# Kernel optimization log

Hardware: AMD Instinct MI355X
Metric: run time of the kernel (lower is better)

The kernel has to match this reference:

```python
import jax, jax.numpy as jnp
import numpy as np

B, N, H, NH, HD, DE = 4, 512, 512, 8, 64, 64
DFF = 4 * H
EPS = 1e-5


def setup_inputs() -> dict:
    key = jax.random.key(0)
    ks = jax.random.split(key, 32)
    w = lambda k, *s: jax.random.normal(k, s, jnp.float32) * 0.02
    inp = {}
    inp['messages'] = jax.random.normal(ks[0], (B, N, H), jnp.float32)
    inp['distance_matrix'] = jax.random.randint(ks[1], (B, N, N), 0, 201).astype(jnp.float32)
    mask = jax.random.randint(ks[2], (B, N, N), 0, 2).astype(jnp.float32)
    inp['mask'] = jnp.maximum(mask, jnp.eye(N, dtype=jnp.float32)[None])  # ensure diag visible
    inp['emb_table'] = w(ks[3], 201, DE)
    inp['Wdq'] = w(ks[4], H, DE); inp['bdq'] = jnp.zeros((H,), jnp.float32)
    inp['Wdk'] = w(ks[5], H, DE); inp['bdk'] = jnp.zeros((H,), jnp.float32)
    inp['Wq'] = w(ks[6], H, H);   inp['bq'] = jnp.zeros((H,), jnp.float32)
    inp['Wk'] = w(ks[7], H, H);   inp['bk'] = jnp.zeros((H,), jnp.float32)
    inp['Wv'] = w(ks[8], H, H);   inp['bv'] = jnp.zeros((H,), jnp.float32)
    inp['Wo'] = w(ks[9], H, H);   inp['bo'] = jnp.zeros((H,), jnp.float32)
    inp['W_ih'] = w(ks[10], 3 * H, H); inp['b_ih'] = jnp.zeros((3 * H,), jnp.float32)
    inp['W_hh'] = w(ks[11], 3 * H, H); inp['b_hh'] = jnp.zeros((3 * H,), jnp.float32)
    inp['W1'] = w(ks[12], DFF, H); inp['b1'] = jnp.zeros((DFF,), jnp.float32)
    inp['W2'] = w(ks[13], H, DFF); inp['b2'] = jnp.zeros((H,), jnp.float32)
    inp['g2'] = jnp.ones((H,), jnp.float32); inp['beta2'] = jnp.zeros((H,), jnp.float32)
    return inp


def reference(messages, distance_matrix, mask, emb_table, Wdq, bdq, Wdk, bdk,
              Wq, bq, Wk, bk, Wv, bv, Wo, bo, W_ih, b_ih, W_hh, b_hh,
              W1, b1, W2, b2, g2, beta2):
    # distance embedding lookup (B,N,N,DE)
    idx = jnp.clip(distance_matrix.astype(jnp.int32), 0, 200)
    emb = emb_table[idx]
    # mean over dim then linear == linear then mean (linear maps commute with mean)
    dq = jnp.mean(emb, axis=2) @ Wdq.T + bdq  # (B,N,H)
    dk = jnp.mean(emb, axis=1) @ Wdk.T + bdk  # (B,N,H)
    Q = ((messages + dq) @ Wq.T + bq).reshape(B, N, NH, HD).transpose(0, 2, 1, 3)
    K = ((messages + dk) @ Wk.T + bk).reshape(B, N, NH, HD).transpose(0, 2, 1, 3)
    V = (messages @ Wv.T + bv).reshape(B, N, NH, HD).transpose(0, 2, 1, 3)
    scale = 1.0 / np.sqrt(HD).astype(np.float32)
    scores = jnp.einsum('bhnd,bhmd->bhnm', Q, K) * scale
    scores = jnp.where(mask[:, None] == 0, -jnp.inf, scores)
    aw = jax.nn.softmax(scores, axis=-1)
    ao = jnp.einsum('bhnm,bhmd->bhnd', aw, V).transpose(0, 2, 1, 3).reshape(B, N, H)
    ao = ao @ Wo.T + bo
    # GRUCell: x = attn output, h = messages
    gx = ao @ W_ih.T + b_ih
    gh = messages @ W_hh.T + b_hh
    xr, xz, xn = jnp.split(gx, 3, axis=-1)
    hr, hz, hn = jnp.split(gh, 3, axis=-1)
    r = jax.nn.sigmoid(xr + hr)
    z = jax.nn.sigmoid(xz + hz)
    n = jnp.tanh(xn + r * hn)
    u = (1.0 - z) * n + z * messages
    # FFN + residual + LayerNorm
    f = jax.nn.relu(u @ W1.T + b1) @ W2.T + b2
    y = u + f
    mu = jnp.mean(y, axis=-1, keepdims=True)
    var = jnp.var(y, axis=-1, keepdims=True)
    return (y - mu) / jnp.sqrt(var + EPS) * g2 + beta2
```

## Files before the change

### kernel.cpp

```cpp
#include <hip/hip_runtime.h>
#include <hip/hip_bf16.h>
#include <math.h>

#define Bz 4
#define Nn 512
#define Hh 512
#define NHh 8
#define HDd 64
#define DEe 64
#define DFFf 2048
#define EPSs 1e-5f
#define QS 1536
#define GS 3072

typedef __attribute__((ext_vector_type(8))) short bf16x8;
typedef __attribute__((ext_vector_type(4))) short bf16x4;
typedef __attribute__((ext_vector_type(4))) float f32x4;

__device__ inline short f2bf(float x) {
    unsigned u = __builtin_bit_cast(unsigned, x);
    unsigned r = (u + 0x7FFFu + ((u >> 16) & 1u)) >> 16;
    return (short)r;
}
__device__ inline float b2f(unsigned short u) {
    unsigned v = ((unsigned)u) << 16;
    return __builtin_bit_cast(float, v);
}
__device__ inline void gld16(const void* g, void* l) {
    __builtin_amdgcn_global_load_lds(
        (const __attribute__((address_space(1))) void*)g,
        (__attribute__((address_space(3))) void*)l, 16, 0, 0);
}

struct CvtArgs {
    const float* src[11];
    unsigned short* dst[11];
    int n[11];
};
__global__ __launch_bounds__(256) void cvttr_kernel(
    CvtArgs a, const float* __restrict__ dist, float* __restrict__ distT)
{
    __shared__ float T[64][68];
    int t = threadIdx.x;
    if (blockIdx.x < 512) {
        for (int sg = 0; sg < 11; ++sg) {
            const float4* s = (const float4*)a.src[sg];
            ushort4* d = (ushort4*)a.dst[sg];
            int n4 = a.n[sg] >> 2;
            for (int i = blockIdx.x * 256 + t; i < n4; i += 512 * 256) {
                float4 v = s[i];
                ushort4 o = {(unsigned short)f2bf(v.x), (unsigned short)f2bf(v.y),
                             (unsigned short)f2bf(v.z), (unsigned short)f2bf(v.w)};
                d[i] = o;
            }
        }
    } else {
        int tid = blockIdx.x - 512;
        int b = tid >> 6;
        int i0 = ((tid >> 3) & 7) * 64, j0 = (tid & 7) * 64;
        int rr = t >> 4, c4 = (t & 15) * 4;
#pragma unroll
        for (int p = 0; p < 4; ++p) {
            int r = rr + p * 16;
            float4 v = *(const float4*)&dist[((size_t)(b * Nn + i0 + r)) * Nn + j0 + c4];
            *(float4*)&T[r][c4] = v;
        }
        __syncthreads();
#pragma unroll
        for (int p = 0; p < 4; ++p) {
            int jr = rr + p * 16;
            float4 v = {T[c4 + 0][jr], T[c4 + 1][jr], T[c4 + 2][jr], T[c4 + 3][jr]};
            *(float4*)&distT[((size_t)(b * Nn + j0 + jr)) * Nn + i0 + c4] = v;
        }
    }
}

__global__ __launch_bounds__(256) void dmean2_kernel(
    const float* __restrict__ dist, const float* __restrict__ distT,
    const float* __restrict__ emb,
    unsigned short* __restrict__ dqe, unsigned short* __restrict__ dke)
{
    int bi = blockIdx.x;
    const float* src = blockIdx.y ? distT : dist;
    unsigned short* out = blockIdx.y ? dke : dqe;
    int t = threadIdx.x;
    int d = t & 63;
    int g = t >> 6;
    const float* drow = src + (size_t)bi * Nn + g * 128;
    float acc = 0.f;
#pragma unroll 4
    for (int it = 0; it < 32; ++it) {
        float4 v = *(const float4*)(drow + it * 4);
        int i0 = min(max((int)v.x, 0), 200);
        int i1 = min(max((int)v.y, 0), 200);
        int i2 = min(max((int)v.z, 0), 200);
        int i3 = min(max((int)v.w, 0), 200);
        acc += emb[i0 * DEe + d];
        acc += emb[i1 * DEe + d];
        acc += emb[i2 * DEe + d];
        acc += emb[i3 * DEe + d];
    }
    __shared__ float red[4][64];
    red[g][d] = acc;
    __syncthreads();
    if (g == 0) {
        float s = red[0][d] + red[1][d] + red[2][d] + red[3][d];
        out[(size_t)bi * DEe + d] = (unsigned short)f2bf(s * (1.0f / Nn));
    }
}

struct SegArgs {
    const unsigned short* A[3];
    int lda[3];
    const float* bias[3];
    const void* res[3];
    int rlda;
};

template<int BM, int BN, int RELU, int RESM, int OUTF>
__global__ __launch_bounds__(256) void mgf_kernel(
    SegArgs sa, const unsigned short* __restrict__ W,
    void* __restrict__ C, int K, int SW, int ldc)
{
    constexpr int WM = BM / 2, WN = BN / 2;
    constexpr int MT = WM / 16, NT = WN / 16;
    constexpr int IPA = BM / 32, IPB = BN / 32;
    __shared__ unsigned short As[2][BM * 64];
    __shared__ unsigned short Bs[2][BN * 64];
    int t = threadIdx.x, lane = t & 63, wid = t >> 6;
    int wm = wid >> 1, wn = wid & 1;
    int m0 = blockIdx.y * BM, n0 = blockIdx.x * BN;
    int seg = n0 / SW;
    int segbase = seg * SW;
    const unsigned short* A = sa.A[seg];
    int lda = sa.lda[seg];
    int lrow8 = lane >> 3;
    int lunit = (lane & 7) ^ lrow8;

    f32x4 acc[MT][NT] = {};

    auto stage = [&](int buf, int kt) {
#pragma unroll
        for (int i = 0; i < IPA; ++i) {
            int c = wid * IPA + i;
            gld16(A + (size_t)(m0 + c * 8 + lrow8) * lda + kt + lunit * 8,
                  &As[buf][c * 512]);
        }
#pragma unroll
        for (int i = 0; i < IPB; ++i) {
            int c = wid * IPB + i;
            gld16(W + (size_t)(n0 + c * 8 + lrow8) * K + kt + lunit * 8,
                  &Bs[buf][c * 512]);
        }
    };

    stage(0, 0);
    __syncthreads();
    int cur = 0;
    for (int kt = 0; kt < K; kt += 64) {
        if (kt + 64 < K) stage(cur ^ 1, kt + 64);
#pragma unroll
        for (int kk = 0; kk < 2; ++kk) {
            bf16x8 fa[MT], fb[NT];
            int ub = kk * 4 + (lane >> 4);
#pragma unroll
            for (int mt = 0; mt < MT; ++mt) {
                int r = wm * WM + mt * 16 + (lane & 15);
                fa[mt] = *(const bf16x8*)&As[cur][r * 64 + ((ub ^ (r & 7)) << 3)];
            }
#pragma unroll
            for (int nt = 0; nt < NT; ++nt) {
                int r = wn * WN + nt * 16 + (lane & 15);
                fb[nt] = *(const bf16x8*)&Bs[cur][r * 64 + ((ub ^ (r & 7)) << 3)];
            }
#pragma unroll
            for (int mt = 0; mt < MT; ++mt)
#pragma unroll
                for (int nt = 0; nt < NT; ++nt)
                    acc[mt][nt] = __builtin_amdgcn_mfma_f32_16x16x32_bf16(
                        fa[mt], fb[nt], acc[mt][nt], 0, 0, 0);
        }
        __syncthreads();
        cur ^= 1;
    }

    int cr = (lane >> 4) * 4, ccl = lane & 15;
#pragma unroll
    for (int mt = 0; mt < MT; ++mt) {
#pragma unroll
        for (int nt = 0; nt < NT; ++nt) {
            int col = n0 + wn * WN + nt * 16 + ccl;
            int lcol = col - segbase;
            float bv = sa.bias[seg][lcol];
#pragma unroll
            for (int r = 0; r < 4; ++r) {
                int row = m0 + wm * WM + mt * 16 + cr + r;
                float o = acc[mt][nt][r] + bv;
                if (RESM == 1)
                    o += ((const float*)sa.res[seg])[(size_t)row * sa.rlda + lcol];
                if (RESM == 2)
                    o += b2f(((const unsigned short*)sa.res[seg])
                                 [(size_t)row * sa.rlda + lcol]);
                if (RELU) o = fmaxf(o, 0.f);
                if (OUTF)
                    ((float*)C)[(size_t)row * ldc + col] = o;
                else
                    ((unsigned short*)C)[(size_t)row * ldc + col] =
                        (unsigned short)f2bf(o);
            }
        }
    }
}

__global__ __launch_bounds__(256) void attn_mfma_kernel(
    const unsigned short* __restrict__ QKV, const float* __restrict__ mask,
    unsigned short* __restrict__ AO)
{
    __shared__ unsigned short Qs[64 * 64];
    __shared__ unsigned short Ks[64 * 64];
    __shared__ unsigned short Vt[64 * 64];
    __shared__ float Ms[64 * 65];
    __shared__ unsigned short Pl[4][16 * 72];

    int t = threadIdx.x;
    int lane = t & 63;
    int wq = t >> 6;
    int g = lane >> 4, cc = lane & 15;
    int q0 = blockIdx.x * 64;
    int h = blockIdx.y, b = blockIdx.z;

    int lr = t >> 2;
    int u0 = (t & 3) * 2;
    int c0f = (t & 3) * 16;

    {
        const unsigned short* src =
            QKV + ((size_t)(b * Nn + q0 + lr)) * QS + h * HDd + u0 * 8;
        bf16x8 p0 = *(const bf16x8*)(src);
        bf16x8 p1 = *(const bf16x8*)(src + 8);
        *(bf16x8*)&Qs[lr * 64 + ((u0 ^ (lr & 7)) << 3)] = p0;
        *(bf16x8*)&Qs[lr * 64 + (((u0 + 1) ^ (lr & 7)) << 3)] = p1;
    }

    const unsigned short* Krow =
        QKV + ((size_t)(b * Nn + lr)) * QS + 512 + h * HDd + u0 * 8;
    int vkey = t >> 4;
    int vd0 = (t & 15) * 4;
    const unsigned short* Vbase =
        QKV + ((size_t)(b * Nn)) * QS + 1024 + h * HDd + vd0;
    const float* Mrow = mask + ((size_t)(b * Nn + q0 + lr)) * Nn + c0f;

    bf16x8 kr0, kr1;
    ushort4 vr[4];
    float4 mreg[4];
    auto issue = [&](int kc) {
        int k0 = kc * 64;
        const unsigned short* kp = Krow + (size_t)k0 * QS;
        kr0 = *(const bf16x8*)(kp);
        kr1 = *(const bf16x8*)(kp + 8);
        const float* mp = Mrow + k0;
        mreg[0] = *(const float4*)(mp);
        mreg[1] = *(const float4*)(mp + 4);
        mreg[2] = *(const float4*)(mp + 8);
        mreg[3] = *(const float4*)(mp + 12);
#pragma unroll
        for (int p = 0; p < 4; ++p)
            vr[p] = *(const ushort4*)(Vbase + (size_t)(k0 + vkey + p * 16) * QS);
    };
    issue(0);
    __syncthreads();

    bf16x8 qf0 = *(bf16x8*)&Qs[(wq * 16 + cc) * 64 + (((0 * 4 + g) ^ (cc & 7)) << 3)];
    bf16x8 qf1 = *(bf16x8*)&Qs[(wq * 16 + cc) * 64 + (((1 * 4 + g) ^ (cc & 7)) << 3)];

    const float scale = 0.125f;
    float m_run = -1e30f, l_run = 0.f;
    f32x4 o[4] = {};

    for (int kc = 0; kc < 8; ++kc) {
        {
            *(bf16x8*)&Ks[lr * 64 + ((u0 ^ (lr & 7)) << 3)] = kr0;
            *(bf16x8*)&Ks[lr * 64 + (((u0 + 1) ^ (lr & 7)) << 3)] = kr1;

            float* msr = &Ms[lr * 65 + c0f];
            msr[0] = mreg[0].x;  msr[1] = mreg[0].y;  msr[2] = mreg[0].z;  msr[3] = mreg[0].w;
            msr[4] = mreg[1].x;  msr[5] = mreg[1].y;  msr[6] = mreg[1].z;  msr[7] = mreg[1].w;
            msr[8] = mreg[2].x;  msr[9] = mreg[2].y;  msr[10] = mreg[2].z; msr[11] = mreg[2].w;
            msr[12] = mreg[3].x; msr[13] = mreg[3].y; msr[14] = mreg[3].z; msr[15] = mreg[3].w;

#pragma unroll
            for (int p = 0; p < 4; ++p) {
                int key = vkey + p * 16;
                unsigned short vals[4] = {vr[p].x, vr[p].y, vr[p].z, vr[p].w};
#pragma unroll
                for (int jj = 0; jj < 4; ++jj) {
                    int j = (jj + (t >> 2)) & 3;
                    int d = vd0 + j;
                    Vt[d * 64 + (key ^ ((d & 7) << 3))] = vals[j];
                }
            }
        }
        __syncthreads();
        if (kc < 7) issue(kc + 1);

        f32x4 s[4] = {};
#pragma unroll
        for (int kt = 0; kt < 4; ++kt) {
            int rA = kt * 16 + cc;
            bf16x8 a0 = *(bf16x8*)&Ks[rA * 64 + (((0 * 4 + g) ^ (rA & 7)) << 3)];
            s[kt] = __builtin_amdgcn_mfma_f32_16x16x32_bf16(a0, qf0, s[kt], 0, 0, 0);
            bf16x8 a1 = *(bf16x8*)&Ks[rA * 64 + (((1 * 4 + g) ^ (rA & 7)) << 3)];
            s[kt] = __builtin_amdgcn_mfma_f32_16x16x32_bf16(a1, qf1, s[kt], 0, 0, 0);
        }

        float pv[4][4];
        float tmax = -1e30f;
#pragma unroll
        for (int kt = 0; kt < 4; ++kt) {
#pragma unroll
            for (int r = 0; r < 4; ++r) {
                float mv = Ms[(wq * 16 + cc) * 65 + kt * 16 + g * 4 + r];
                float svv = (mv == 0.f) ? -1e30f : s[kt][r];
                pv[kt][r] = svv;
                tmax = fmaxf(tmax, svv);
            }
        }
        tmax = fmaxf(tmax, __shfl_xor(tmax, 16));
        tmax = fmaxf(tmax, __shfl_xor(tmax, 32));
        float mnew = fmaxf(m_run, tmax);
        float rescale = __expf((m_run - mnew) * scale);
        float psum = 0.f;
#pragma unroll
        for (int kt = 0; kt < 4; ++kt) {
#pragma unroll
            for (int r = 0; r < 4; ++r) {
                float sv = pv[kt][r];
                float p = (sv == -1e30f) ? 0.f : __expf((sv - mnew) * scale);
                pv[kt][r] = p;
                psum += p;
            }
        }
        psum += __shfl_xor(psum, 16);
        psum += __shfl_xor(psum, 32);
        l_run = l_run * rescale + psum;
        m_run = mnew;
#pragma unroll
        for (int dt = 0; dt < 4; ++dt) {
            o[dt][0] *= rescale; o[dt][1] *= rescale;
            o[dt][2] *= rescale; o[dt][3] *= rescale;
        }

#pragma unroll
        for (int kt = 0; kt < 4; ++kt) {
            bf16x4 pk = {f2bf(pv[kt][0]), f2bf(pv[kt][1]),
                         f2bf(pv[kt][2]), f2bf(pv[kt][3])};
            *(bf16x4*)&Pl[wq][cc * 72 + kt * 16 + g * 4] = pk;
        }
        bf16x8 pf0 = *(bf16x8*)&Pl[wq][cc * 72 + 0 + g * 8];
        bf16x8 pf1 = *(bf16x8*)&Pl[wq][cc * 72 + 32 + g * 8];

#pragma unroll
        for (int dt = 0; dt < 4; ++dt) {
            int rV = dt * 16 + cc;
            bf16x8 vf0 = *(bf16x8*)&Vt[rV * 64 + (((0 * 4 + g) ^ (rV & 7)) << 3)];
            o[dt] = __builtin_amdgcn_mfma_f32_16x16x32_bf16(vf0, pf0, o[dt], 0, 0, 0);
            bf16x8 vf1 = *(bf16x8*)&Vt[rV * 64 + (((1 * 4 + g) ^ (rV & 7)) << 3)];
            o[dt] = __builtin_amdgcn_mfma_f32_16x16x32_bf16(vf1, pf1, o[dt], 0, 0, 0);
        }
        __syncthreads();
    }

    float invl = 1.f / l_run;
#pragma unroll
    for (int dt = 0; dt < 4; ++dt) {
        ushort4 w = {(unsigned short)f2bf(o[dt][0] * invl),
                     (unsigned short)f2bf(o[dt][1] * invl),
                     (unsigned short)f2bf(o[dt][2] * invl),
                     (unsigned short)f2bf(o[dt][3] * invl)};
        *(ushort4*)&AO[((size_t)(b * Nn + q0 + wq * 16 + cc)) * Hh +
                       h * HDd + dt * 16 + g * 4] = w;
    }
}

__global__ __launch_bounds__(256) void gru_kernel(
    const unsigned short* __restrict__ G,
    const float* __restrict__ msg, unsigned short* __restrict__ u)
{
    int i4 = blockIdx.x * 256 + threadIdx.x;
    int e = i4 * 4;
    int row = e >> 9, col = e & 511;
    const unsigned short* gxr = G + (size_t)row * GS;
    const unsigned short* ghr = gxr + 1536;
    ushort4 xr4 = *(const ushort4*)(gxr + col);
    ushort4 xz4 = *(const ushort4*)(gxr + col + 512);
    ushort4 xn4 = *(const ushort4*)(gxr + col + 1024);
    ushort4 hr4 = *(const ushort4*)(ghr + col);
    ushort4 hz4 = *(const ushort4*)(ghr + col + 512);
    ushort4 hn4 = *(const ushort4*)(ghr + col + 1024);
    float4 mg4 = *(const float4*)(msg + e);
    float mv[4] = {mg4.x, mg4.y, mg4.z, mg4.w};
    unsigned short xr[4] = {xr4.x, xr4.y, xr4.z, xr4.w};
    unsigned short xz[4] = {xz4.x, xz4.y, xz4.z, xz4.w};
    unsigned short xn[4] = {xn4.x, xn4.y, xn4.z, xn4.w};
    unsigned short hr[4] = {hr4.x, hr4.y, hr4.z, hr4.w};
    unsigned short hz[4] = {hz4.x, hz4.y, hz4.z, hz4.w};
    unsigned short hn[4] = {hn4.x, hn4.y, hn4.z, hn4.w};
    ushort4 out;
    unsigned short* op = (unsigned short*)&out;
#pragma unroll
    for (int j = 0; j < 4; ++j) {
        float r = 1.f / (1.f + __expf(-(b2f(xr[j]) + b2f(hr[j]))));
        float z = 1.f / (1.f + __expf(-(b2f(xz[j]) + b2f(hz[j]))));
        float n = tanhf(b2f(xn[j]) + r * b2f(hn[j]));
        op[j] = (unsigned short)f2bf((1.f - z) * n + z * mv[j]);
    }
    *(ushort4*)(u + e) = out;
}

__global__ __launch_bounds__(256) void ln_kernel(
    const float* __restrict__ Y, const float* __restrict__ g,
    const float* __restrict__ be, float* __restrict__ out)
{
    int row = blockIdx.x, t = threadIdx.x;
    const float* yr = Y + (size_t)row * Hh;
    float v0 = yr[t], v1 = yr[t + 256];
    float s = v0 + v1, s2 = v0 * v0 + v1 * v1;
#pragma unroll
    for (int o = 1; o < 64; o <<= 1) {
        s += __shfl_xor(s, o);
        s2 += __shfl_xor(s2, o);
    }
    __shared__ float rs[4], rs2[4];
    int w = t >> 6;
    if ((t & 63) == 0) { rs[w] = s; rs2[w] = s2; }
    __syncthreads();
    float ts = rs[0] + rs[1] + rs[2] + rs[3];
    float ts2 = rs2[0] + rs2[1] + rs2[2] + rs2[3];
    float mu = ts * (1.0f / Hh);
    float var = ts2 * (1.0f / Hh) - mu * mu;
    float rstd = rsqrtf(var + EPSs);
    out[(size_t)row * Hh + t] = (v0 - mu) * rstd * g[t] + be[t];
    out[(size_t)row * Hh + t + 256] = (v1 - mu) * rstd * g[t + 256] + be[t + 256];
}

extern "C" void kernel_launch(void* const* d_in, const int* in_sizes, int n_in,
                              void* d_out, int out_size, void* d_ws, size_t ws_size,
                              hipStream_t stream) {
    const float* messages = (const float*)d_in[0];
    const float* dist     = (const float*)d_in[1];
    const float* mask     = (const float*)d_in[2];
    const float* emb      = (const float*)d_in[3];
    const float* Wdq = (const float*)d_in[4];  const float* bdq = (const float*)d_in[5];
    const float* Wdk = (const float*)d_in[6];  const float* bdk = (const float*)d_in[7];
    const float* Wq  = (const float*)d_in[8];  const float* bq  = (const float*)d_in[9];
    const float* Wk  = (const float*)d_in[10]; const float* bk  = (const float*)d_in[11];
    const float* Wv  = (const float*)d_in[12]; const float* bv  = (const float*)d_in[13];
    const float* Wo  = (const float*)d_in[14]; const float* bo  = (const float*)d_in[15];
    const float* W_ih = (const float*)d_in[16]; const float* b_ih = (const float*)d_in[17];
    const float* W_hh = (const float*)d_in[18]; const float* b_hh = (const float*)d_in[19];
    const float* W1  = (const float*)d_in[20]; const float* b1  = (const float*)d_in[21];
    const float* W2  = (const float*)d_in[22]; const float* b2  = (const float*)d_in[23];
    const float* g2  = (const float*)d_in[24]; const float* beta2 = (const float*)d_in[25];

    const int M = Bz * Nn;
    char* ws = (char*)d_ws;

    unsigned short* wdqb = (unsigned short*)(ws + 0);
    unsigned short* wdkb = (unsigned short*)(ws + 65536);
    unsigned short* wqkv = (unsigned short*)(ws + 131072);
    unsigned short* wob  = (unsigned short*)(ws + 1703936);
    unsigned short* wgate= (unsigned short*)(ws + 2228224);
    unsigned short* w1b  = (unsigned short*)(ws + 5373952);
    unsigned short* w2b  = (unsigned short*)(ws + 7471104);
    unsigned short* msgs = (unsigned short*)(ws + 9568256);
    unsigned short* dqe  = (unsigned short*)(ws + 11665408);
    unsigned short* dke  = (unsigned short*)(ws + 11927552);
    unsigned short* XQXK = (unsigned short*)(ws + 12189696);
    unsigned short* QKVb = (unsigned short*)(ws + 16384000);
    unsigned short* AO   = (unsigned short*)(ws + 22675456);
    unsigned short* aob  = (unsigned short*)(ws + 24772608);
    unsigned short* G    = (unsigned short*)(ws + 26869760);
    unsigned short* ub   = (unsigned short*)(ws + 39452672);
    unsigned short* f1   = (unsigned short*)(ws + 41549824);
    float*          yb   = (float*)(ws + 49938432);
    float*          distT= (float*)(ws + 54132736);

    dim3 blk(256);

    CvtArgs ca;
    ca.src[0] = messages; ca.dst[0] = msgs; ca.n[0] = M * Hh;
    ca.src[1] = Wdq;  ca.dst[1] = wdqb;          ca.n[1] = Hh * DEe;
    ca.src[2] = Wdk;  ca.dst[2] = wdkb;          ca.n[2] = Hh * DEe;
    ca.src[3] = Wq;   ca.dst[3] = wqkv;          ca.n[3] = Hh * Hh;
    ca.src[4] = Wk;   ca.dst[4] = wqkv + 262144; ca.n[4] = Hh * Hh;
    ca.src[5] = Wv;   ca.dst[5] = wqkv + 524288; ca.n[5] = Hh * Hh;
    ca.src[6] = Wo;   ca.dst[6] = wob;           ca.n[6] = Hh * Hh;
    ca.src[7] = W_ih; ca.dst[7] = wgate;         ca.n[7] = 3 * Hh * Hh;
    ca.src[8] = W_hh; ca.dst[8] = wgate + 786432;ca.n[8] = 3 * Hh * Hh;
    ca.src[9] = W1;   ca.dst[9] = w1b;           ca.n[9] = DFFf * Hh;
    ca.src[10] = W2;  ca.dst[10] = w2b;          ca.n[10] = Hh * DFFf;
    cvttr_kernel<<<768, blk, 0, stream>>>(ca, dist, distT);

    dmean2_kernel<<<dim3(M, 2), blk, 0, stream>>>(dist, distT, emb, dqe, dke);

    {
        SegArgs sa = {};
        sa.A[0] = dqe; sa.A[1] = dke; sa.lda[0] = 64; sa.lda[1] = 64;
        sa.bias[0] = bdq; sa.bias[1] = bdk;
        sa.res[0] = messages; sa.res[1] = messages; sa.rlda = Hh;
        mgf_kernel<128, 64, 0, 1, 0><<<dim3(16, 16), blk, 0, stream>>>(
            sa, wdqb, XQXK, DEe, 512, 1024);
    }

    {
        SegArgs sa = {};
        sa.A[0] = XQXK; sa.A[1] = XQXK + 512; sa.A[2] = msgs;
        sa.lda[0] = 1024; sa.lda[1] = 1024; sa.lda[2] = 512;
        sa.bias[0] = bq; sa.bias[1] = bk; sa.bias[2] = bv;
        mgf_kernel<64, 128, 0, 0, 0><<<dim3(12, 32), blk, 0, stream>>>(
            sa, wqkv, QKVb, Hh, 512, QS);
    }

    attn_mfma_kernel<<<dim3(Nn / 64, NHh, Bz), blk, 0, stream>>>(
        QKVb, mask, AO);

    {
        SegArgs sa = {};
        sa.A[0] = AO; sa.lda[0] = 512; sa.bias[0] = bo;
        mgf_kernel<64, 64, 0, 0, 0><<<dim3(8, 32), blk, 0, stream>>>(
            sa, wob, aob, Hh, 512, 512);
    }

    {
        SegArgs sa = {};
        sa.A[0] = aob; sa.A[1] = msgs; sa.lda[0] = 512; sa.lda[1] = 512;
        sa.bias[0] = b_ih; sa.bias[1] = b_hh;
        mgf_kernel<128, 128, 0, 0, 0><<<dim3(24, 16), blk, 0, stream>>>(
            sa, wgate, G, Hh, 1536, GS);
    }
    gru_kernel<<<(M * Hh) / 1024, blk, 0, stream>>>(G, messages, ub);

    {
        SegArgs sa = {};
        sa.A[0] = ub; sa.lda[0] = 512; sa.bias[0] = b1;
        mgf_kernel<128, 128, 1, 0, 0><<<dim3(16, 16), blk, 0, stream>>>(
            sa, w1b, f1, Hh, 2048, DFFf);
    }
    {
        SegArgs sa = {};
        sa.A[0] = f1; sa.lda[0] = 2048; sa.bias[0] = b2;
        sa.res[0] = ub; sa.rlda = 512;
        mgf_kernel<64, 64, 0, 2, 1><<<dim3(8, 32), blk, 0, stream>>>(
            sa, w2b, yb, DFFf, 512, 512);
    }

    ln_kernel<<<M, blk, 0, stream>>>(yb, g2, beta2, (float*)d_out);
}
```

Before: 144.6 us.

## Replace embedding gather-mean with distance histogram GEMM against projected table

The per-row gather of embedding rows and its mean are replaced by a 256-bin histogram of clipped distances per row, built with shared-memory atomics. A small GEMM projects the scaled embedding table through Wdq into Ecat, and the distance projection then becomes histogram × Ecat with K=256 instead of K=64. This removes 512 scattered embedding reads per row, at the cost of a bf16 histogram, one extra GEMM launch and a larger K. Separately, s_setprio is raised around the MFMA blocks in the attention kernel, and a HASB template flag is added to the GEMM so it can run without a bias.

```diff
diff --git a/kernel.cpp b/kernel.cpp
--- a/kernel.cpp
+++ b/kernel.cpp
@@ -38,7 +38,8 @@
     int n[11];
 };
 __global__ __launch_bounds__(256) void cvttr_kernel(
-    CvtArgs a, const float* __restrict__ dist, float* __restrict__ distT)
+    CvtArgs a, const float* __restrict__ dist, float* __restrict__ distT,
+    const float* __restrict__ emb, unsigned short* __restrict__ embb)
 {
     __shared__ float T[64][68];
     int t = threadIdx.x;
@@ -54,6 +55,18 @@
                 d[i] = o;
             }
         }
+        const float sc = 1.0f / 512.0f;
+        for (int i = blockIdx.x * 256 + t; i < 4096; i += 512 * 256) {
+            ushort4 o = {0, 0, 0, 0};
+            if (i * 4 < 201 * 64) {
+                float4 v = *(const float4*)(emb + i * 4);
+                o.x = (unsigned short)f2bf(v.x * sc);
+                o.y = (unsigned short)f2bf(v.y * sc);
+                o.z = (unsigned short)f2bf(v.z * sc);
+                o.w = (unsigned short)f2bf(v.w * sc);
+            }
+            *(ushort4*)(embb + i * 4) = o;
+        }
     } else {
         int tid = blockIdx.x - 512;
         int b = tid >> 6;
@@ -75,38 +88,24 @@
     }
 }
 
-__global__ __launch_bounds__(256) void dmean2_kernel(
+__global__ __launch_bounds__(256) void hist2_kernel(
     const float* __restrict__ dist, const float* __restrict__ distT,
-    const float* __restrict__ emb,
-    unsigned short* __restrict__ dqe, unsigned short* __restrict__ dke)
+    unsigned short* __restrict__ histq, unsigned short* __restrict__ histk)
 {
+    __shared__ int hist[256];
     int bi = blockIdx.x;
     const float* src = blockIdx.y ? distT : dist;
-    unsigned short* out = blockIdx.y ? dke : dqe;
+    unsigned short* out = blockIdx.y ? histk : histq;
     int t = threadIdx.x;
-    int d = t & 63;
-    int g = t >> 6;
-    const float* drow = src + (size_t)bi * Nn + g * 128;
-    float acc = 0.f;
-#pragma unroll 4
-    for (int it = 0; it < 32; ++it) {
-        float4 v = *(const float4*)(drow + it * 4);
-        int i0 = min(max((int)v.x, 0), 200);
-        int i1 = min(max((int)v.y, 0), 200);
-        int i2 = min(max((int)v.z, 0), 200);
-        int i3 = min(max((int)v.w, 0), 200);
-        acc += emb[i0 * DEe + d];
-        acc += emb[i1 * DEe + d];
-        acc += emb[i2 * DEe + d];
-        acc += emb[i3 * DEe + d];
-    }
-    __shared__ float red[4][64];
-    red[g][d] = acc;
+    hist[t] = 0;
     __syncthreads();
-    if (g == 0) {
-        float s = red[0][d] + red[1][d] + red[2][d] + red[3][d];
-        out[(size_t)bi * DEe + d] = (unsigned short)f2bf(s * (1.0f / Nn));
-    }
+    float2 v = *(const float2*)(src + (size_t)bi * Nn + t * 2);
+    int i0 = min(max((int)v.x, 0), 200);
+    int i1 = min(max((int)v.y, 0), 200);
+    atomicAdd(&hist[i0], 1);
+    atomicAdd(&hist[i1], 1);
+    __syncthreads();
+    out[(size_t)bi * 256 + t] = (unsigned short)f2bf((float)hist[t]);
 }
 
 struct SegArgs {
@@ -117,7 +116,7 @@
     int rlda;
 };
 
-template<int BM, int BN, int RELU, int RESM, int OUTF>
+template<int BM, int BN, int RELU, int RESM, int OUTF, int HASB>
 __global__ __launch_bounds__(256) void mgf_kernel(
     SegArgs sa, const unsigned short* __restrict__ W,
     void* __restrict__ C, int K, int SW, int ldc)
@@ -191,7 +190,7 @@
         for (int nt = 0; nt < NT; ++nt) {
             int col = n0 + wn * WN + nt * 16 + ccl;
             int lcol = col - segbase;
-            float bv = sa.bias[seg][lcol];
+            float bv = HASB ? sa.bias[seg][lcol] : 0.f;
 #pragma unroll
             for (int r = 0; r < 4; ++r) {
                 int row = m0 + wm * WM + mt * 16 + cr + r;
@@ -304,6 +303,7 @@
         if (kc < 7) issue(kc + 1);
 
         f32x4 s[4] = {};
+        __builtin_amdgcn_s_setprio(1);
 #pragma unroll
         for (int kt = 0; kt < 4; ++kt) {
             int rA = kt * 16 + cc;
@@ -312,6 +312,7 @@
             bf16x8 a1 = *(bf16x8*)&Ks[rA * 64 + (((1 * 4 + g) ^ (rA & 7)) << 3)];
             s[kt] = __builtin_amdgcn_mfma_f32_16x16x32_bf16(a1, qf1, s[kt], 0, 0, 0);
         }
+        __builtin_amdgcn_s_setprio(0);
 
         float pv[4][4];
         float tmax = -1e30f;
@@ -359,6 +360,7 @@
         bf16x8 pf0 = *(bf16x8*)&Pl[wq][cc * 72 + 0 + g * 8];
         bf16x8 pf1 = *(bf16x8*)&Pl[wq][cc * 72 + 32 + g * 8];
 
+        __builtin_amdgcn_s_setprio(1);
 #pragma unroll
         for (int dt = 0; dt < 4; ++dt) {
             int rV = dt * 16 + cc;
@@ -367,6 +369,7 @@
             bf16x8 vf1 = *(bf16x8*)&Vt[rV * 64 + (((1 * 4 + g) ^ (rV & 7)) << 3)];
             o[dt] = __builtin_amdgcn_mfma_f32_16x16x32_bf16(vf1, pf1, o[dt], 0, 0, 0);
         }
+        __builtin_amdgcn_s_setprio(0);
         __syncthreads();
     }
 
@@ -473,8 +476,6 @@
     unsigned short* w1b  = (unsigned short*)(ws + 5373952);
     unsigned short* w2b  = (unsigned short*)(ws + 7471104);
     unsigned short* msgs = (unsigned short*)(ws + 9568256);
-    unsigned short* dqe  = (unsigned short*)(ws + 11665408);
-    unsigned short* dke  = (unsigned short*)(ws + 11927552);
     unsigned short* XQXK = (unsigned short*)(ws + 12189696);
     unsigned short* QKVb = (unsigned short*)(ws + 16384000);
     unsigned short* AO   = (unsigned short*)(ws + 22675456);
@@ -484,6 +485,10 @@
     unsigned short* f1   = (unsigned short*)(ws + 41549824);
     float*          yb   = (float*)(ws + 49938432);
     float*          distT= (float*)(ws + 54132736);
+    unsigned short* embb = (unsigned short*)(ws + 58327040);
+    unsigned short* histq= (unsigned short*)(ws + 58359808);
+    unsigned short* histk= (unsigned short*)(ws + 59408384);
+    unsigned short* Ecat = (unsigned short*)(ws + 60456960);
 
     dim3 blk(256);
 
@@ -499,17 +504,24 @@
     ca.src[8] = W_hh; ca.dst[8] = wgate + 786432;ca.n[8] = 3 * Hh * Hh;
     ca.src[9] = W1;   ca.dst[9] = w1b;           ca.n[9] = DFFf * Hh;
     ca.src[10] = W2;  ca.dst[10] = w2b;          ca.n[10] = Hh * DFFf;
-    cvttr_kernel<<<768, blk, 0, stream>>>(ca, dist, distT);
-
-    dmean2_kernel<<<dim3(M, 2), blk, 0, stream>>>(dist, distT, emb, dqe, dke);
-
-    {
-        SegArgs sa = {};
-        sa.A[0] = dqe; sa.A[1] = dke; sa.lda[0] = 64; sa.lda[1] = 64;
+    cvttr_kernel<<<768, blk, 0, stream>>>(ca, dist, distT, emb, embb);
+
+    hist2_kernel<<<dim3(M, 2), blk, 0, stream>>>(dist, distT, histq, histk);
+
+    {
+        SegArgs sa = {};
+        sa.A[0] = wdqb; sa.lda[0] = 64;
+        mgf_kernel<128, 64, 0, 0, 0, 0><<<dim3(4, 8), blk, 0, stream>>>(
+            sa, embb, Ecat, 64, 256, 256);
+    }
+
+    {
+        SegArgs sa = {};
+        sa.A[0] = histq; sa.A[1] = histk; sa.lda[0] = 256; sa.lda[1] = 256;
         sa.bias[0] = bdq; sa.bias[1] = bdk;
         sa.res[0] = messages; sa.res[1] = messages; sa.rlda = Hh;
-        mgf_kernel<128, 64, 0, 1, 0><<<dim3(16, 16), blk, 0, stream>>>(
-            sa, wdqb, XQXK, DEe, 512, 1024);
+        mgf_kernel<128, 64, 0, 1, 0, 1><<<dim3(16, 16), blk, 0, stream>>>(
+            sa, Ecat, XQXK, 256, 512, 1024);
     }
 
     {
@@ -517,7 +529,7 @@
         sa.A[0] = XQXK; sa.A[1] = XQXK + 512; sa.A[2] = msgs;
         sa.lda[0] = 1024; sa.lda[1] = 1024; sa.lda[2] = 512;
         sa.bias[0] = bq; sa.bias[1] = bk; sa.bias[2] = bv;
-        mgf_kernel<64, 128, 0, 0, 0><<<dim3(12, 32), blk, 0, stream>>>(
+        mgf_kernel<64, 128, 0, 0, 0, 1><<<dim3(12, 32), blk, 0, stream>>>(
             sa, wqkv, QKVb, Hh, 512, QS);
     }
 
@@ -527,7 +539,7 @@
     {
         SegArgs sa = {};
         sa.A[0] = AO; sa.lda[0] = 512; sa.bias[0] = bo;
-        mgf_kernel<64, 64, 0, 0, 0><<<dim3(8, 32), blk, 0, stream>>>(
+        mgf_kernel<64, 64, 0, 0, 0, 1><<<dim3(8, 32), blk, 0, stream>>>(
             sa, wob, aob, Hh, 512, 512);
     }
 
@@ -535,7 +547,7 @@
         SegArgs sa = {};
         sa.A[0] = aob; sa.A[1] = msgs; sa.lda[0] = 512; sa.lda[1] = 512;
         sa.bias[0] = b_ih; sa.bias[1] = b_hh;
-        mgf_kernel<128, 128, 0, 0, 0><<<dim3(24, 16), blk, 0, stream>>>(
+        mgf_kernel<128, 128, 0, 0, 0, 1><<<dim3(24, 16), blk, 0, stream>>>(
             sa, wgate, G, Hh, 1536, GS);
     }
     gru_kernel<<<(M * Hh) / 1024, blk, 0, stream>>>(G, messages, ub);
@@ -543,14 +555,14 @@
     {
         SegArgs sa = {};
         sa.A[0] = ub; sa.lda[0] = 512; sa.bias[0] = b1;
-        mgf_kernel<128, 128, 1, 0, 0><<<dim3(16, 16), blk, 0, stream>>>(
+        mgf_kernel<128, 128, 1, 0, 0, 1><<<dim3(16, 16), blk, 0, stream>>>(
             sa, w1b, f1, Hh, 2048, DFFf);
     }
     {
         SegArgs sa = {};
         sa.A[0] = f1; sa.lda[0] = 2048; sa.bias[0] = b2;
         sa.res[0] = ub; sa.rlda = 512;
-        mgf_kernel<64, 64, 0, 2, 1><<<dim3(8, 32), blk, 0, stream>>>(
+        mgf_kernel<64, 64, 0, 2, 1, 1><<<dim3(8, 32), blk, 0, stream>>>(
             sa, w2b, yb, DFFf, 512, 512);
     }
 
```

After: 123.5 us. -14.6%, faster.
